# Kernel optimization log

Measured on AMD Instinct MI355X. Metric: run time of the kernel, lower is better.

## Reference

```python
import jax, jax.numpy as jnp
import numpy as np

B, Q, T, H, V = 8, 1, 2048, 512, 32000


def setup_inputs() -> dict:
    key = jax.random.key(0)
    k0, k1, k2, k3, k4 = jax.random.split(key, 5)
    s1 = 1.0 / np.sqrt(2 * H)
    return {
        "input_embeds": jax.random.normal(k0, (B, Q, H), dtype=jnp.float32),
        "target_embeds": jax.random.normal(k1, (B, T, H), dtype=jnp.float32),
        "input_mask": jnp.ones((B, T), dtype=jnp.float32),
        # MLP params: l1 Linear(2H->H, bias), l2 Linear(H->1, no bias)
        "w1": (jax.random.normal(k2, (H, 2 * H), dtype=jnp.float32) * s1),
        "b1": jnp.zeros((H,), dtype=jnp.float32),
        "w2": (jax.random.normal(k3, (H,), dtype=jnp.float32) * (1.0 / np.sqrt(H))),
        # decoder: Linear(H->V, no bias) -> weight [V, H]
        "decoder_weight": (jax.random.normal(k4, (V, H), dtype=jnp.float32) * 0.02),
    }


def reference(input_embeds, target_embeds, input_mask, w1, b1, w2, decoder_weight):
    h = w1.shape[0]
    # l1(cat(q, t)) == q @ W1q^T + t @ W1t^T + b1  (split first linear)
    w1q, w1t = w1[:, :h], w1[:, h:]
    q_proj = jnp.einsum('bqh,kh->bqk', input_embeds, w1q)        # [B,Q,H]
    t_proj = jnp.einsum('bth,kh->btk', target_embeds, w1t)       # [B,T,H]
    # pairwise query x target MLP scoring
    ht = jax.nn.relu(q_proj[:, :, None, :] + t_proj[:, None, :, :] + b1)  # [B,Q,T,H]
    repair_logits = jnp.einsum('bqtk,k->bqt', ht, w2)             # [B,Q,T]
    # _mask: mask*logits - 1000*(1-mask); mask [B,T] -> [B,1,T]
    mask = input_mask[:, None, :]
    repair_logits = mask * repair_logits - 1000.0 * (1.0 - mask)
    # decoder branch: query x vocab-row MLP scoring
    d_proj = jnp.einsum('vh,kh->vk', decoder_weight, w1t)         # [V,H]
    hd = jax.nn.relu(q_proj[:, :, None, :] + d_proj[None, None, :, :] + b1)  # [B,Q,V,H]
    decoder_logits = jnp.einsum('bqvk,k->bqv', hd, w2)            # [B,Q,V]
    out = jnp.concatenate([decoder_logits, repair_logits], axis=2)  # [B,Q,V+T]
    return jnp.squeeze(out, axis=1)  # Q == 1 -> [B, V+T]
```

## Files before the change

### kernel.cpp

```cpp
#include <hip/hip_runtime.h>
#include <hip/hip_bf16.h>

#define Hdim 512
#define Bdim 8
#define Tdim 2048
#define Vdim 32000
#define OUTW (Vdim + Tdim)
#define DEC_TILES (Vdim / 128)
#define REP_TILES ((Bdim * Tdim) / 128)
#define NTILES (DEC_TILES + REP_TILES)

typedef __attribute__((ext_vector_type(8))) short short8;
typedef __attribute__((ext_vector_type(16))) float f32x16;

__device__ __forceinline__ unsigned packbf2(float a, float b) {
    __hip_bfloat162 h = __float22bfloat162_rn(make_float2(a, b));
    union { __hip_bfloat162 h; unsigned u; } c; c.h = h;
    return c.u;
}

union U8 { unsigned u[4]; short8 s; };
__device__ __forceinline__ short8 cvt8(const float4 f0, const float4 f1) {
    U8 r;
    r.u[0] = packbf2(f0.x, f0.y); r.u[1] = packbf2(f0.z, f0.w);
    r.u[2] = packbf2(f1.x, f1.y); r.u[3] = packbf2(f1.z, f1.w);
    return r.s;
}

#define WT_BLOCKS 128
#define QP_BLOCKS (Bdim * Hdim / 4)
#define INIT_BLOCKS (Bdim * OUTW / 4 / 256)

__global__ __launch_bounds__(256) void prep_kernel(
    const float* __restrict__ w1, const float* __restrict__ x,
    const float* __restrict__ b1, const float* __restrict__ mask,
    unsigned short* __restrict__ wt, float* __restrict__ qp,
    float* __restrict__ out)
{
    const int bid = blockIdx.x;
    if (bid < WT_BLOCKS) {
        const int i = bid * 256 + threadIdx.x;
        const int n = i >> 6;
        const int kk = (i & 63) * 8;
        const float4* s = (const float4*)(w1 + (size_t)n * 1024 + 512 + kk);
        const float4 v0 = s[0], v1 = s[1];
        uint4 o;
        o.x = packbf2(v0.x, v0.y); o.y = packbf2(v0.z, v0.w);
        o.z = packbf2(v1.x, v1.y); o.w = packbf2(v1.z, v1.w);
        ((uint4*)wt)[i] = o;
    } else if (bid < WT_BLOCKS + QP_BLOCKS) {
        const int widx = (bid - WT_BLOCKS) * 4 + (threadIdx.x >> 6);
        const int lane = threadIdx.x & 63;
        const int b = widx >> 9, k = widx & 511;
        const float4* xr = (const float4*)(x + b * Hdim);
        const float4* wr = (const float4*)(w1 + (size_t)k * 1024);
        float4 x0 = xr[lane * 2], x1 = xr[lane * 2 + 1];
        float4 w0 = wr[lane * 2], w1v = wr[lane * 2 + 1];
        float s = x0.x * w0.x + x0.y * w0.y + x0.z * w0.z + x0.w * w0.w
                + x1.x * w1v.x + x1.y * w1v.y + x1.z * w1v.z + x1.w * w1v.w;
#pragma unroll
        for (int off = 32; off > 0; off >>= 1) s += __shfl_down(s, off);
        if (lane == 0) qp[b * Hdim + k] = s + b1[k];
    } else {
        const int idx4 = (bid - WT_BLOCKS - QP_BLOCKS) * 256 + threadIdx.x;
        const int b = idx4 / (OUTW / 4);
        const int c4 = (idx4 - b * (OUTW / 4)) * 4;
        float4 v;
        if (c4 < Vdim) {
            v = make_float4(0.f, 0.f, 0.f, 0.f);
        } else {
            const int t = c4 - Vdim;
            const float4 mv = *(const float4*)(mask + b * Tdim + t);
            v = make_float4(-1000.f * (1.f - mv.x), -1000.f * (1.f - mv.y),
                            -1000.f * (1.f - mv.z), -1000.f * (1.f - mv.w));
        }
        ((float4*)out)[idx4] = v;
    }
}

__global__ __launch_bounds__(256, 3) void gemm_kernel(
    const float* __restrict__ Adec,
    const float* __restrict__ Atgt,
    const unsigned short* __restrict__ Wt,
    const float* __restrict__ qp,
    const float* __restrict__ w2,
    const float* __restrict__ mask,
    float* __restrict__ out)
{
    __shared__ union {
        struct { float A[2][64][64]; unsigned short W[2][64][64]; } g;
        struct { float qT[8][128]; float w2c[128]; } e;
    } u;

    const int tid  = threadIdx.x;
    const int lane = tid & 63;
    const int w    = tid >> 6;

    const int b = blockIdx.x;
    const int mt = (b >> 5) * 8 + (b & 7);
    if (mt >= NTILES) return;
    const int chunk = (b >> 3) & 3;
    const int n0 = chunk << 7;
    const bool is_dec = (mt < DEC_TILES);
    const int m0 = (is_dec ? mt : mt - DEC_TILES) << 7;
    const float* __restrict__ Af = is_dec ? Adec : Atgt;

    const float* gAp[4];
#pragma unroll
    for (int j = 0; j < 4; ++j) {
        const int rr = w * 16 + j * 4 + (lane >> 4);
        const int lc = (lane & 15) ^ (rr & 15);
        gAp[j] = Af + (size_t)(m0 + rr + 64 * (lc >> 3)) * 512 + (lc & 7) * 4;
    }
    const unsigned short* gWp[2];
    {
        const int lcw = (lane & 7) ^ (lane >> 3);
#pragma unroll
        for (int j = 0; j < 2; ++j) {
            const int rr = w * 16 + j * 8 + (lane >> 3);
            gWp[j] = Wt + (size_t)(n0 + rr + 64 * (lcw >> 2)) * 512 + (lcw & 3) * 8;
        }
    }

#define STAGE(bb, koff) do {                                                  \
        _Pragma("unroll")                                                     \
        for (int j = 0; j < 4; ++j)                                           \
            __builtin_amdgcn_global_load_lds(                                 \
                (const __attribute__((address_space(1))) unsigned int*)(gAp[j] + (koff)), \
                (__attribute__((address_space(3))) unsigned int*)(&u.g.A[bb][w * 16 + j * 4][0]), \
                16, 0, 0);                                                    \
        _Pragma("unroll")                                                     \
        for (int j = 0; j < 2; ++j)                                           \
            __builtin_amdgcn_global_load_lds(                                 \
                (const __attribute__((address_space(1))) unsigned int*)(gWp[j] + (koff)), \
                (__attribute__((address_space(3))) unsigned int*)(&u.g.W[bb][w * 16 + j * 8][0]), \
                16, 0, 0);                                                    \
    } while (0)

    f32x16 acc00, acc01, acc10, acc11;
#pragma unroll
    for (int i = 0; i < 16; ++i) { acc00[i] = 0.f; acc01[i] = 0.f; acc10[i] = 0.f; acc11[i] = 0.f; }

    const int wm  = (w & 1) << 6;
    const int wn  = (w >> 1) << 6;
    const int l31 = lane & 31;
    const int kh  = lane >> 5;
    const int rx15 = l31 & 15;
    const int rx7  = l31 & 7;
    const int ha  = wm >> 6;
    const int hw  = wn >> 6;

    STAGE(0, 0);
    __syncthreads();

    int cur = 0;
    for (int t = 0; t < 16; ++t) {
        if (t < 15) STAGE(cur ^ 1, (t + 1) * 32);
        const float (* __restrict__ Ab)[64] = u.g.A[cur];
        const unsigned short (* __restrict__ Wb)[64] = u.g.W[cur];
#pragma unroll
        for (int s = 0; s < 2; ++s) {
            const int g  = s * 2 + kh;
            const int p0 = ((ha * 8 + 2 * g) ^ rx15) << 2;
            const int p1 = ((ha * 8 + 2 * g + 1) ^ rx15) << 2;
            const float4 a0f0 = *(const float4*)&Ab[l31][p0];
            const float4 a0f1 = *(const float4*)&Ab[l31][p1];
            const float4 a1f0 = *(const float4*)&Ab[l31 + 32][p0];
            const float4 a1f1 = *(const float4*)&Ab[l31 + 32][p1];
            const short8 a0 = cvt8(a0f0, a0f1);
            const short8 a1 = cvt8(a1f0, a1f1);
            const int ow = ((hw * 4 + g) ^ rx7) << 3;
            const short8 b0 = *(const short8*)&Wb[l31][ow];
            const short8 b1 = *(const short8*)&Wb[l31 + 32][ow];
            acc00 = __builtin_amdgcn_mfma_f32_32x32x16_bf16(b0, a0, acc00, 0, 0, 0);
            acc01 = __builtin_amdgcn_mfma_f32_32x32x16_bf16(b0, a1, acc01, 0, 0, 0);
            acc10 = __builtin_amdgcn_mfma_f32_32x32x16_bf16(b1, a0, acc10, 0, 0, 0);
            acc11 = __builtin_amdgcn_mfma_f32_32x32x16_bf16(b1, a1, acc11, 0, 0, 0);
        }
        __syncthreads();
        cur ^= 1;
    }
#undef STAGE

    {
        const int qb = tid >> 5;
        const int qn = (tid & 31) << 2;
        *(float4*)&u.e.qT[qb][qn] = *(const float4*)&qp[qb * Hdim + n0 + qn];
        if (tid < 32) *(float4*)&u.e.w2c[tid << 2] = *(const float4*)&w2[n0 + (tid << 2)];
    }
    __syncthreads();

    const int kh4 = kh << 2;

    float4 wvA[4], wvB[4];
#pragma unroll
    for (int run = 0; run < 4; ++run) {
        wvA[run] = *(const float4*)&u.e.w2c[wn + run * 8 + kh4];
        wvB[run] = *(const float4*)&u.e.w2c[wn + 32 + run * 8 + kh4];
    }

#define EPI_PAIR(QROW, T0, T1) do {                                          \
        float _p0 = 0.f, _p1 = 0.f;                                          \
        _Pragma("unroll")                                                    \
        for (int run = 0; run < 4; ++run) {                                  \
            const float4 q0 = *(const float4*)((QROW) + wn + run * 8 + kh4); \
            const float4 q1 = *(const float4*)((QROW) + wn + 32 + run * 8 + kh4); \
            const float4 wA = wvA[run], wB = wvB[run];                       \
            _p0 += fmaxf(acc00[run * 4 + 0] + q0.x, 0.f) * wA.x;             \
            _p1 += fmaxf(acc01[run * 4 + 0] + q0.x, 0.f) * wA.x;             \
            _p0 += fmaxf(acc10[run * 4 + 0] + q1.x, 0.f) * wB.x;             \
            _p1 += fmaxf(acc11[run * 4 + 0] + q1.x, 0.f) * wB.x;             \
            _p0 += fmaxf(acc00[run * 4 + 1] + q0.y, 0.f) * wA.y;             \
            _p1 += fmaxf(acc01[run * 4 + 1] + q0.y, 0.f) * wA.y;             \
            _p0 += fmaxf(acc10[run * 4 + 1] + q1.y, 0.f) * wB.y;             \
            _p1 += fmaxf(acc11[run * 4 + 1] + q1.y, 0.f) * wB.y;             \
            _p0 += fmaxf(acc00[run * 4 + 2] + q0.z, 0.f) * wA.z;             \
            _p1 += fmaxf(acc01[run * 4 + 2] + q0.z, 0.f) * wA.z;             \
            _p0 += fmaxf(acc10[run * 4 + 2] + q1.z, 0.f) * wB.z;             \
            _p1 += fmaxf(acc11[run * 4 + 2] + q1.z, 0.f) * wB.z;             \
            _p0 += fmaxf(acc00[run * 4 + 3] + q0.w, 0.f) * wA.w;             \
            _p1 += fmaxf(acc01[run * 4 + 3] + q0.w, 0.f) * wA.w;             \
            _p0 += fmaxf(acc10[run * 4 + 3] + q1.w, 0.f) * wB.w;             \
            _p1 += fmaxf(acc11[run * 4 + 3] + q1.w, 0.f) * wB.w;             \
        }                                                                    \
        T0 = _p0 + __shfl_xor(_p0, 32);                                      \
        T1 = _p1 + __shfl_xor(_p1, 32);                                      \
    } while (0)

    if (is_dec) {
#pragma unroll
        for (int b2 = 0; b2 < 8; ++b2) {
            float t0, t1;
            EPI_PAIR(&u.e.qT[b2][0], t0, t1);
            if (kh == 0) {
                float* o = out + (size_t)b2 * OUTW + m0 + wm;
                unsafeAtomicAdd(o + l31, t0);
                unsafeAtomicAdd(o + 32 + l31, t1);
            }
        }
    } else {
        const int bfix = m0 >> 11;
        float t0, t1;
        EPI_PAIR(&u.e.qT[bfix][0], t0, t1);
        if (kh == 0) {
            const int t0i = (m0 & 2047) + wm + l31;
            const int t1i = t0i + 32;
            const float mv0 = mask[bfix * Tdim + t0i];
            const float mv1 = mask[bfix * Tdim + t1i];
            float* o = out + (size_t)bfix * OUTW + Vdim;
            unsafeAtomicAdd(o + t0i, mv0 * t0);
            unsafeAtomicAdd(o + t1i, mv1 * t1);
        }
    }
#undef EPI_PAIR
}

extern "C" void kernel_launch(void* const* d_in, const int* in_sizes, int n_in,
                              void* d_out, int out_size, void* d_ws, size_t ws_size,
                              hipStream_t stream) {
    const float* input_embeds  = (const float*)d_in[0];
    const float* target_embeds = (const float*)d_in[1];
    const float* input_mask    = (const float*)d_in[2];
    const float* w1            = (const float*)d_in[3];
    const float* b1            = (const float*)d_in[4];
    const float* w2            = (const float*)d_in[5];
    const float* decoder_w     = (const float*)d_in[6];
    float* out = (float*)d_out;

    float* qp = (float*)d_ws;
    unsigned short* wt = (unsigned short*)((char*)d_ws + 16384);

    prep_kernel<<<WT_BLOCKS + QP_BLOCKS + INIT_BLOCKS, 256, 0, stream>>>(
        w1, input_embeds, b1, input_mask, wt, qp, out);
    gemm_kernel<<<48 * 32, 256, 0, stream>>>(
        decoder_w, target_embeds, wt, qp, w2, input_mask, out);
}
```

Before: 173.2 us.

## Convert A tile to bf16 once at staging instead of per-wave in LDS reads

The fp32 activation tile now goes into registers through ordinary global loads and is converted to bf16 once per element before being written to LDS. Previously each wave reread fp32 from LDS and converted it on every MFMA step, which duplicated conversions across waves. The LDS layout changes to a k-major [32][128] bf16 arrangement with a new XOR swizzle, which halves LDS footprint and read traffic for A. The trade-off is that A no longer uses asynchronous global-to-LDS DMA, so the loads occupy VGPRs and must finish before the post-compute convert-and-store step.

Measured after the change: 188.4 us. 1.09x slower.

```diff
diff --git a/kernel.cpp b/kernel.cpp
--- a/kernel.cpp
+++ b/kernel.cpp
@@ -88,7 +88,7 @@
     float* __restrict__ out)
 {
     __shared__ union {
-        struct { float A[2][64][64]; unsigned short W[2][64][64]; } g;
+        struct { unsigned short A[2][32][128]; unsigned short W[2][32][128]; } g;
         struct { float qT[8][128]; float w2c[128]; } e;
     } u;
 
@@ -105,35 +105,38 @@
     const int m0 = (is_dec ? mt : mt - DEC_TILES) << 7;
     const float* __restrict__ Af = is_dec ? Adec : Atgt;
 
-    const float* gAp[4];
-#pragma unroll
-    for (int j = 0; j < 4; ++j) {
-        const int rr = w * 16 + j * 4 + (lane >> 4);
-        const int lc = (lane & 15) ^ (rr & 15);
-        gAp[j] = Af + (size_t)(m0 + rr + 64 * (lc >> 3)) * 512 + (lc & 7) * 4;
-    }
+    const int sr  = tid >> 1;
+    const float* gAr = Af + (size_t)(m0 + sr) * 512 + ((tid & 1) << 4);
+    const int awr = sr & 31;
+    const int as0 = ((sr >> 5) << 2) + ((tid & 1) << 1);
+    const int ap0 = ((as0)     ^ (sr & 15)) << 3;
+    const int ap1 = ((as0 + 1) ^ (sr & 15)) << 3;
+
     const unsigned short* gWp[2];
-    {
-        const int lcw = (lane & 7) ^ (lane >> 3);
-#pragma unroll
-        for (int j = 0; j < 2; ++j) {
-            const int rr = w * 16 + j * 8 + (lane >> 3);
-            gWp[j] = Wt + (size_t)(n0 + rr + 64 * (lcw >> 2)) * 512 + (lcw & 3) * 8;
-        }
-    }
-
-#define STAGE(bb, koff) do {                                                  \
-        _Pragma("unroll")                                                     \
-        for (int j = 0; j < 4; ++j)                                           \
-            __builtin_amdgcn_global_load_lds(                                 \
-                (const __attribute__((address_space(1))) unsigned int*)(gAp[j] + (koff)), \
-                (__attribute__((address_space(3))) unsigned int*)(&u.g.A[bb][w * 16 + j * 4][0]), \
-                16, 0, 0);                                                    \
+#pragma unroll
+    for (int j = 0; j < 2; ++j) {
+        const int rr = (w * 2 + j) * 4 + (lane >> 4);
+        const int s  = (lane & 15) ^ (rr & 15);
+        gWp[j] = Wt + (size_t)(n0 + (s >> 2) * 32 + rr) * 512 + (s & 3) * 8;
+    }
+
+    float4 rA0, rA1, rA2, rA3;
+#define GLOAD_A(kof) do {                                                     \
+        rA0 = *(const float4*)(gAr + (kof));                                  \
+        rA1 = *(const float4*)(gAr + (kof) + 4);                              \
+        rA2 = *(const float4*)(gAr + (kof) + 8);                              \
+        rA3 = *(const float4*)(gAr + (kof) + 12);                             \
+    } while (0)
+#define CVT_A(bb) do {                                                        \
+        *(short8*)&u.g.A[bb][awr][ap0] = cvt8(rA0, rA1);                      \
+        *(short8*)&u.g.A[bb][awr][ap1] = cvt8(rA2, rA3);                      \
+    } while (0)
+#define STAGE_W(bb, kof) do {                                                 \
         _Pragma("unroll")                                                     \
         for (int j = 0; j < 2; ++j)                                           \
             __builtin_amdgcn_global_load_lds(                                 \
-                (const __attribute__((address_space(1))) unsigned int*)(gWp[j] + (koff)), \
-                (__attribute__((address_space(3))) unsigned int*)(&u.g.W[bb][w * 16 + j * 8][0]), \
+                (const __attribute__((address_space(1))) unsigned int*)(gWp[j] + (kof)), \
+                (__attribute__((address_space(3))) unsigned int*)(&u.g.W[bb][(w * 2 + j) * 4][0]), \
                 16, 0, 0);                                                    \
     } while (0)
 
@@ -146,41 +149,45 @@
     const int l31 = lane & 31;
     const int kh  = lane >> 5;
     const int rx15 = l31 & 15;
-    const int rx7  = l31 & 7;
-    const int ha  = wm >> 6;
-    const int hw  = wn >> 6;
-
-    STAGE(0, 0);
+    const int ca  = wm >> 5;
+    const int cw  = wn >> 5;
+
+#define COMPUTE(bb) do {                                                      \
+        _Pragma("unroll")                                                     \
+        for (int s = 0; s < 2; ++s) {                                         \
+            const int g = s * 2 + kh;                                         \
+            const short8 a0 = *(const short8*)&u.g.A[bb][l31][(((ca)*4 + g) ^ rx15) << 3];     \
+            const short8 a1 = *(const short8*)&u.g.A[bb][l31][(((ca+1)*4 + g) ^ rx15) << 3];   \
+            const short8 b0 = *(const short8*)&u.g.W[bb][l31][(((cw)*4 + g) ^ rx15) << 3];     \
+            const short8 b1 = *(const short8*)&u.g.W[bb][l31][(((cw+1)*4 + g) ^ rx15) << 3];   \
+            acc00 = __builtin_amdgcn_mfma_f32_32x32x16_bf16(b0, a0, acc00, 0, 0, 0); \
+            acc01 = __builtin_amdgcn_mfma_f32_32x32x16_bf16(b0, a1, acc01, 0, 0, 0); \
+            acc10 = __builtin_amdgcn_mfma_f32_32x32x16_bf16(b1, a0, acc10, 0, 0, 0); \
+            acc11 = __builtin_amdgcn_mfma_f32_32x32x16_bf16(b1, a1, acc11, 0, 0, 0); \
+        }                                                                     \
+    } while (0)
+
+    GLOAD_A(0);
+    STAGE_W(0, 0);
+    CVT_A(0);
     __syncthreads();
 
     int cur = 0;
     for (int t = 0; t < 16; ++t) {
-        if (t < 15) STAGE(cur ^ 1, (t + 1) * 32);
-        const float (* __restrict__ Ab)[64] = u.g.A[cur];
-        const unsigned short (* __restrict__ Wb)[64] = u.g.W[cur];
-#pragma unroll
-        for (int s = 0; s < 2; ++s) {
-            const int g  = s * 2 + kh;
-            const int p0 = ((ha * 8 + 2 * g) ^ rx15) << 2;
-            const int p1 = ((ha * 8 + 2 * g + 1) ^ rx15) << 2;
-            const float4 a0f0 = *(const float4*)&Ab[l31][p0];
-            const float4 a0f1 = *(const float4*)&Ab[l31][p1];
-            const float4 a1f0 = *(const float4*)&Ab[l31 + 32][p0];
-            const float4 a1f1 = *(const float4*)&Ab[l31 + 32][p1];
-            const short8 a0 = cvt8(a0f0, a0f1);
-            const short8 a1 = cvt8(a1f0, a1f1);
-            const int ow = ((hw * 4 + g) ^ rx7) << 3;
-            const short8 b0 = *(const short8*)&Wb[l31][ow];
-            const short8 b1 = *(const short8*)&Wb[l31 + 32][ow];
-            acc00 = __builtin_amdgcn_mfma_f32_32x32x16_bf16(b0, a0, acc00, 0, 0, 0);
-            acc01 = __builtin_amdgcn_mfma_f32_32x32x16_bf16(b0, a1, acc01, 0, 0, 0);
-            acc10 = __builtin_amdgcn_mfma_f32_32x32x16_bf16(b1, a0, acc10, 0, 0, 0);
-            acc11 = __builtin_amdgcn_mfma_f32_32x32x16_bf16(b1, a1, acc11, 0, 0, 0);
-        }
+        if (t < 15) {
+            GLOAD_A((t + 1) * 32);
+            STAGE_W(cur ^ 1, (t + 1) * 32);
+        }
+        COMPUTE(cur);
+        if (t < 15) CVT_A(cur ^ 1);
         __syncthreads();
         cur ^= 1;
     }
-#undef STAGE
+
+#undef COMPUTE
+#undef GLOAD_A
+#undef CVT_A
+#undef STAGE_W
 
     {
         const int qb = tid >> 5;
```
